# Kernel tuning notes

Measured on AMD Instinct MI355X. Metric: run time of the kernel, lower is better.

Reference implementation:

```python
import jax, jax.numpy as jnp
import numpy as np

T = 22        # TypeEncoder.tensor_size() (assumed)
H = 2         # attention heads
C = 64        # hc_graph (per-head out channels)
L = 3         # num_hops
LEAFCAT = 5   # len(LeafType.valid_categories()) (assumed)
NSIZES = 8    # len(LeafType.valid_sizes()) (assumed)
HL = 64       # hc_linear
HT = 64       # hc_task == hc_leafsize
SLOPE = 0.2   # PyG GATConv negative_slope


def _gat(x, src, dst, W, asrc, adst, b):
    # PyG GATConv (concat=True, dropout=0, self-loops already appended to src/dst)
    N = x.shape[0]
    h = (x @ W).reshape(N, H, C)                      # [N,H,C]
    a_s = jnp.einsum('nhc,hc->nh', h, asrc)            # per-node src score
    a_d = jnp.einsum('nhc,hc->nh', h, adst)            # per-node dst score
    e = jax.nn.leaky_relu(a_s[src] + a_d[dst], SLOPE)  # [E+N,H]
    m = jax.ops.segment_max(e, dst, num_segments=N)
    p = jnp.exp(e - m[dst])
    s = jax.ops.segment_sum(p, dst, num_segments=N)
    alpha = p / (s[dst] + 1e-16)                       # scatter-softmax over in-edges
    out = jax.ops.segment_sum(h[src] * alpha[:, :, None], dst, num_segments=N)
    return out.reshape(N, H * C) + b


def _mlp2(z, W1, b1, W2, b2):
    return jax.nn.relu(z @ W1 + b1) @ W2 + b2


def setup_inputs() -> dict:
    key = jax.random.key(0)
    ks = jax.random.split(key, 32)
    N, E, NG, NPG = 102400, 1228800, 256, 400
    D = H * C
    g = lambda k, shp, fan: (jax.random.normal(k, shp, jnp.float32) / np.sqrt(fan)).astype(jnp.float32)
    z = lambda *shp: jnp.zeros(shp, jnp.float32)
    return {
        'x': jax.random.normal(ks[0], (N, D), jnp.float32),
        'edge_index': jax.random.randint(ks[1], (2, E), 0, N),
        'batch': jnp.repeat(jnp.arange(NG, dtype=jnp.int32), NPG),
        'gat_W': g(ks[2], (L, D, D), D),
        'gat_asrc': g(ks[3], (L, H, C), C),
        'gat_adst': g(ks[4], (L, H, C), C),
        'gat_b': z(L, D),
        'shared_W': g(ks[5], (D + T, HL), D + T),
        'shared_b': z(HL),
        'ptr_W1': g(ks[6], (3, HL, HT), HL), 'ptr_b1': z(3, HT),
        'ptr_W2': g(ks[7], (3, HT, 3), HT), 'ptr_b2': z(3, 3),
        'cat_W1': g(ks[8], (HL, HT), HL), 'cat_b1': z(HT),
        'cat_W2': g(ks[9], (HT, LEAFCAT), HT), 'cat_b2': z(LEAFCAT),
        'sf_W1': g(ks[10], (2, HL, HT), HL), 'sf_b1': z(2, HT),
        'sf_W2': g(ks[11], (2, HT, 1), HT), 'sf_b2': z(2, 1),
        'bool_W1': g(ks[12], (HL + T + LEAFCAT + 2, HT), HL + T + LEAFCAT + 2), 'bool_b1': z(HT),
        'bool_W2': g(ks[13], (HT, 1), HT), 'bool_b2': z(1),
        'size_W1': g(ks[14], (HL + T + LEAFCAT + 3, HT), HL + T + LEAFCAT + 3), 'size_b1': z(HT),
        'size_W2': g(ks[15], (HT, NSIZES), HT), 'size_b2': z(NSIZES),
    }


def reference(x, edge_index, batch, gat_W, gat_asrc, gat_adst, gat_b,
              shared_W, shared_b, ptr_W1, ptr_b1, ptr_W2, ptr_b2,
              cat_W1, cat_b1, cat_W2, cat_b2, sf_W1, sf_b1, sf_W2, sf_b2,
              bool_W1, bool_b1, bool_W2, bool_b2, size_W1, size_b1, size_W2, size_b2):
    N = x.shape[0]
    num_graphs = int(batch[-1]) + 1                    # batch is sorted per-graph ids
    node0 = jnp.searchsorted(batch, jnp.arange(num_graphs))  # first node of each graph
    dtype_vec = x[node0, :T]                           # NodeEncoder.split_node_vec dtype slice
    loops = jnp.arange(N)
    src = jnp.concatenate([edge_index[0], loops])      # GATConv add_self_loops=True
    dst = jnp.concatenate([edge_index[1], loops])
    h = x
    for l in range(L):
        h = _gat(h, src, dst, gat_W[l], gat_asrc[l], gat_adst[l], gat_b[l])
        if l < L - 1:
            h = jax.nn.relu(h)
    zf = jax.nn.relu(jnp.concatenate([h[node0], dtype_vec], axis=1) @ shared_W + shared_b)
    # 3 pointer heads, batched
    p = jax.nn.relu(jnp.einsum('gh,khd->kgd', zf, ptr_W1) + ptr_b1[:, None, :])
    ptr = jnp.einsum('kgd,kdo->kgo', p, ptr_W2) + ptr_b2[:, None, :]
    cat_logits = _mlp2(zf, cat_W1, cat_b1, cat_W2, cat_b2)
    q = jax.nn.relu(jnp.einsum('gh,khd->kgd', zf, sf_W1) + sf_b1[:, None, :])
    sf = jnp.einsum('kgd,kdo->kgo', q, sf_W2) + sf_b2[:, None, :]
    signed, floating = sf[0], sf[1]
    bool_in = jnp.concatenate([zf, dtype_vec, cat_logits, signed, floating], axis=1)
    bool_logit = _mlp2(bool_in, bool_W1, bool_b1, bool_W2, bool_b2)
    size_in = jnp.concatenate([bool_in, bool_logit], axis=1)
    size_logits = _mlp2(size_in, size_W1, size_b1, size_W2, size_b2)
    return (ptr[0], ptr[1], ptr[2], cat_logits, signed, floating, bool_logit, size_logits)
```

## Files before the change

### kernel.cpp

```cpp
#include <hip/hip_runtime.h>
#include <hip/hip_bf16.h>

typedef __hip_bfloat16 bf16;
typedef __attribute__((ext_vector_type(8))) short short8;
typedef __attribute__((ext_vector_type(4))) float floatx4;

#define MF(a, b, c) __builtin_amdgcn_mfma_f32_16x16x32_bf16(a, b, c, 0, 0, 0)
#define ADJ_SLOTS 128

__device__ __forceinline__ float b2f(bf16 v) { return __bfloat162float(v); }
__device__ __forceinline__ unsigned short f2us(float f) {
    bf16 h = __float2bfloat16(f);
    return *(unsigned short*)&h;
}
__device__ __forceinline__ float lo2f(unsigned hv) { return __uint_as_float(hv << 16); }
__device__ __forceinline__ float hi2f(unsigned hv) { return __uint_as_float(hv & 0xffff0000u); }
__device__ __forceinline__ float leaky(float v) { return v > 0.f ? v : 0.2f * v; }

__device__ __forceinline__ float ldw(const void* p, size_t i, int f32) {
    return f32 ? ((const float*)p)[i] : b2f(((const bf16*)p)[i]);
}

template <int F32>
__device__ __forceinline__ float LDWt(const void* p, size_t i) {
    return F32 ? ((const float*)p)[i] : b2f(((const bf16*)p)[i]);
}

__device__ __forceinline__ void quadred(float part[4]) {
#pragma unroll
    for (int m = 1; m <= 8; m <<= 1)
#pragma unroll
        for (int r = 0; r < 4; r++) part[r] += __shfl_xor(part[r], m);
}

__global__ void k_detect_zero(const void* x, int* flagd, char* zbase, size_t zbytes,
                              const int* __restrict__ batch, int* __restrict__ node0,
                              unsigned char* __restrict__ rootb,
                              unsigned char* __restrict__ flag2, int N, int zBlocks) {
    int b = blockIdx.x;
    int t = threadIdx.x;
    if (b == 0) {
        __shared__ int sbad;
        if (t == 0) sbad = 0;
        __syncthreads();
        const bf16* xb = (const bf16*)x;
        int bad = 0;
#pragma unroll
        for (int j = 0; j < 16; j++) {
            float v = b2f(xb[t * 16 + j]);
            if (!(fabsf(v) < 1e10f)) bad = 1;
        }
        if (bad) sbad = 1;
        __syncthreads();
        if (t == 0) flagd[0] = sbad;
    } else if (b < 1 + zBlocks) {
        size_t off = (size_t)(b - 1) * 4096 + (size_t)t * 16;
        if (off < zbytes) *(uint4*)(zbase + off) = make_uint4(0u, 0u, 0u, 0u);
    } else {
        int i = (b - 1 - zBlocks) * 256 + t;
        if (i < N) {
            int bb = batch[i];
            int isroot = (i == 0) || (batch[i - 1] != bb);
            rootb[i] = (unsigned char)isroot;
            flag2[i] = (unsigned char)isroot;
            if (isroot) node0[bb] = i;
        }
    }
}

__global__ void k_prep(const void* __restrict__ x, unsigned short* __restrict__ Ab,
                       int nvec,
                       const void* __restrict__ gw, unsigned short* __restrict__ Wt,
                       const void* as_, const void* ad_, const void* b_,
                       float* asF, float* adF, float* bF,
                       const void* sW_, const void* pW1_, const void* cW1_,
                       const void* fW1_, const void* bW1_, const void* zW1_,
                       unsigned short* __restrict__ Whd,
                       const int* __restrict__ ei, const unsigned char* __restrict__ rootb,
                       unsigned char* __restrict__ flag2, int E,
                       const int* __restrict__ flagd, int nbE) {
    int b = blockIdx.x;
    int t = threadIdx.x;
    if (b < nbE) {
        int e = b * 256 + t;
        if (e < E && rootb[ei[E + e]]) flag2[ei[e]] = 1;
        return;
    }
    int f32 = *flagd;
    b -= nbE;
    if (b < 192) {
        int i = b * 256 + t;
        int l = i >> 14, rem = i & 16383, n = rem >> 7, k = rem & 127;
        Wt[i] = f2us(ldw(gw, (size_t)l * 16384 + (size_t)k * 128 + n, f32));
    } else if (b < 194) {
        int i = (b - 192) * 256 + t;
        if (i < 384) {
            asF[i] = ldw(as_, i, f32);
            adF[i] = ldw(ad_, i, f32);
            bF[i] = ldw(b_, i, f32);
        }
    } else if (b < 194 + 184) {
        int i = (b - 194) * 256 + t;
        float v;
        if (i < 10240) {
            int n = i / 160, k = i - n * 160;
            v = (k < 150) ? ldw(sW_, (size_t)k * 64 + n, f32) : 0.f;
        } else if (i < 22528) {
            int j = i - 10240;
            int kk = j >> 12, r = j & 4095, n = r >> 6, k = r & 63;
            v = ldw(pW1_, (size_t)kk * 4096 + (size_t)k * 64 + n, f32);
        } else if (i < 26624) {
            int j = i - 22528;
            int n = j >> 6, k = j & 63;
            v = ldw(cW1_, (size_t)k * 64 + n, f32);
        } else if (i < 34816) {
            int j = i - 26624;
            int kk = j >> 12, r = j & 4095, n = r >> 6, k = r & 63;
            v = ldw(fW1_, (size_t)kk * 4096 + (size_t)k * 64 + n, f32);
        } else if (i < 40960) {
            int j = i - 34816;
            int n = j / 96, k = j - n * 96;
            v = (k < 93) ? ldw(bW1_, (size_t)k * 64 + n, f32) : 0.f;
        } else {
            int j = i - 40960;
            int n = j / 96, k = j - n * 96;
            v = (k < 94) ? ldw(zW1_, (size_t)k * 64 + n, f32) : 0.f;
        }
        Whd[i] = f2us(v);
    } else {
        if (!f32) return;
        int i = (b - 194 - 184) * 256 + t;
        if (i < nvec) {
            float4 a = ((const float4*)x)[2 * i];
            float4 c = ((const float4*)x)[2 * i + 1];
            uint4 o;
            o.x = ((unsigned)f2us(a.y) << 16) | f2us(a.x);
            o.y = ((unsigned)f2us(a.w) << 16) | f2us(a.z);
            o.z = ((unsigned)f2us(c.y) << 16) | f2us(c.x);
            o.w = ((unsigned)f2us(c.w) << 16) | f2us(c.z);
            ((uint4*)Ab)[i] = o;
        }
    }
}

__global__ void k_scan2lane(const unsigned char* __restrict__ flag1,
                            const unsigned char* __restrict__ flag2,
                            int* __restrict__ wp1, int* __restrict__ wp2,
                            int* __restrict__ bsums, int* __restrict__ nact,
                            int* __restrict__ done, int n, int nb) {
    __shared__ int s[256];
    __shared__ int s2[512];
    __shared__ int lastFlag;
    int tid = threadIdx.x;
    int i = blockIdx.x * 256 + tid;
#pragma unroll
    for (int a = 0; a < 2; a++) {
        int v = 0;
        if (i < n) v = a == 0 ? (int)flag1[i] : (int)flag2[i];
        s[tid] = v;
        __syncthreads();
        for (int d = 1; d < 256; d <<= 1) {
            int t2 = (tid >= d) ? s[tid - d] : 0;
            __syncthreads();
            s[tid] += t2;
            __syncthreads();
        }
        int incl = s[tid];
        if (i < n) {
            if (a == 0) wp1[i] = incl - v;
            else wp2[i] = incl - v;
        }
        if (tid == 255) bsums[a * 512 + blockIdx.x] = incl;
        __syncthreads();
    }
    __threadfence();
    if (tid == 0) lastFlag = (atomicAdd(done, 1) == nb - 1);
    __syncthreads();
    if (!lastFlag) return;
    __threadfence();
#pragma unroll
    for (int a = 0; a < 2; a++) {
        int* arr = bsums + a * 512;
        int v0 = (tid < nb) ? arr[tid] : 0;
        int v1 = (tid + 256 < nb) ? arr[tid + 256] : 0;
        s2[tid] = v0;
        s2[tid + 256] = v1;
        __syncthreads();
        for (int d = 1; d < 512; d <<= 1) {
            int a0 = (tid >= d) ? s2[tid - d] : 0;
            int a1 = (tid + 256 >= d) ? s2[tid + 256 - d] : 0;
            __syncthreads();
            s2[tid] += a0;
            s2[tid + 256] += a1;
            __syncthreads();
        }
        arr[tid] = s2[tid] - v0;
        arr[tid + 256] = s2[tid + 256] - v1;
        if (tid == 255) nact[a] = s2[511];
        __syncthreads();
    }
}

__global__ void k_scatter_wl(const int* __restrict__ ei,
                             int* __restrict__ cur,
                             const unsigned char* __restrict__ flag1,
                             const unsigned char* __restrict__ flag2,
                             const int* __restrict__ wp1, const int* __restrict__ wp2,
                             const int* __restrict__ bsums,
                             int* __restrict__ adj,
                             int* __restrict__ ovfD, int* __restrict__ ovfS,
                             int* __restrict__ ovfCnt,
                             int* __restrict__ wl1, int* __restrict__ wl2,
                             int E, int N, int eBlocks) {
    int b = blockIdx.x;
    if (b < eBlocks) {
        int e = b * 256 + threadIdx.x;
        if (e >= E) return;
        int d = ei[E + e];
        if (!flag1[d]) return;
        int slot = atomicAdd(&cur[d], 1);
        if (slot < ADJ_SLOTS) {
            adj[(size_t)d * ADJ_SLOTS + slot] = ei[e];
        } else {
            int o = atomicAdd(ovfCnt, 1);
            if (o < E) { ovfD[o] = d; ovfS[o] = ei[e]; }
        }
    } else {
        int i = (b - eBlocks) * 256 + threadIdx.x;
        if (i < N) {
            if (flag1[i]) wl1[wp1[i] + bsums[i >> 8]] = i;
            if (flag2[i]) wl2[wp2[i] + bsums[512 + (i >> 8)]] = i;
        }
    }
}

__device__ __forceinline__ void gemm_body(
    const unsigned short* __restrict__ Asrc, const unsigned short* __restrict__ Wt,
    unsigned short* __restrict__ Bb, float4* __restrict__ asadv,
    const float* __restrict__ asF, const float* __restrict__ adF, int N,
    const int* __restrict__ wl, const int* __restrict__ nactp,
    int bb0, int bstride) {
    __shared__ __align__(16) unsigned short Ws[128 * 136];
    __shared__ __align__(16) unsigned short Cs[64 * 136];

    int t = threadIdx.x;
    int nact = wl ? *nactp : N;
    if (bb0 * 64 >= nact) return;

    {
        const uint4* src = (const uint4*)Wt;
#pragma unroll
        for (int k = 0; k < 8; k++) {
            int j = t + k * 256;
            int row = j >> 4, c16 = j & 15;
            *(uint4*)&Ws[row * 136 + c16 * 8] = src[j];
        }
    }
    __syncthreads();

    int lane = t & 63;
    int w = t >> 6;
    int ln = lane & 15;
    int quad = lane >> 4;

    for (int bb = bb0; bb * 64 < nact; bb += bstride) {
        int r0 = bb * 64;
        int idx = r0 + w * 16 + ln;
        bool valid = idx < nact;
        int arow = idx < N ? idx : N - 1;
        if (wl) arow = valid ? wl[idx] : 0;
        bool wave_active = __any((int)valid);

        if (wave_active) {
            const unsigned short* ap = Asrc + (size_t)arow * 128 + quad * 8;

            short8 afrag[4];
            if (valid) {
#pragma unroll
                for (int kt = 0; kt < 4; kt++)
                    afrag[kt] = *(const short8*)(ap + kt * 32);
            } else {
#pragma unroll
                for (int kt = 0; kt < 4; kt++)
                    afrag[kt] = (short8){0, 0, 0, 0, 0, 0, 0, 0};
            }

            floatx4 acc[8];
#pragma unroll
            for (int nt = 0; nt < 8; nt++) acc[nt] = (floatx4){0.f, 0.f, 0.f, 0.f};

#pragma unroll
            for (int nt = 0; nt < 8; nt++) {
                const unsigned short* wp = Ws + (nt * 16 + ln) * 136 + quad * 8;
#pragma unroll
                for (int kt = 0; kt < 4; kt++) {
                    short8 bfrag = *(const short8*)(wp + kt * 32);
                    acc[nt] = MF(afrag[kt], bfrag, acc[nt]);
                }
            }

            float as0[4] = {0, 0, 0, 0}, as1[4] = {0, 0, 0, 0};
            float ad0[4] = {0, 0, 0, 0}, ad1[4] = {0, 0, 0, 0};
#pragma unroll
            for (int nt = 0; nt < 8; nt++) {
                float asc = asF[nt * 16 + ln];
                float adc = adF[nt * 16 + ln];
#pragma unroll
                for (int r = 0; r < 4; r++) {
                    float v = acc[nt][r];
                    Cs[(w * 16 + quad * 4 + r) * 136 + nt * 16 + ln] = f2us(v);
                    if (nt < 4) { as0[r] += v * asc; ad0[r] += v * adc; }
                    else        { as1[r] += v * asc; ad1[r] += v * adc; }
                }
            }
#pragma unroll
            for (int mask = 1; mask <= 8; mask <<= 1) {
#pragma unroll
                for (int r = 0; r < 4; r++) {
                    as0[r] += __shfl_xor(as0[r], mask);
                    as1[r] += __shfl_xor(as1[r], mask);
                    ad0[r] += __shfl_xor(ad0[r], mask);
                    ad1[r] += __shfl_xor(ad1[r], mask);
                }
            }
            if (ln == 0) {
#pragma unroll
                for (int r = 0; r < 4; r++) {
                    int idx3 = r0 + w * 16 + quad * 4 + r;
                    if (idx3 < nact) {
                        int row = wl ? wl[idx3] : idx3;
                        asadv[row] = make_float4(as0[r], as1[r], ad0[r], ad1[r]);
                    }
                }
            }
        }
        __syncthreads();

        {
            int idx2 = r0 + (t >> 2);
            int cseg = (t & 3) * 32;
            if (idx2 < nact) {
                int grow = wl ? wl[idx2] : idx2;
                const short8* srcp = (const short8*)&Cs[(t >> 2) * 136 + cseg];
                short8* dstp = (short8*)&Bb[(size_t)grow * 128 + cseg];
#pragma unroll
                for (int u = 0; u < 4; u++) dstp[u] = srcp[u];
            }
        }
        __syncthreads();
    }
}

__global__ __launch_bounds__(256) void k_gemm_mfma(
    const unsigned short* __restrict__ Ab, const unsigned short* __restrict__ Wt,
    unsigned short* __restrict__ Bb, float4* __restrict__ asadv,
    const float* __restrict__ asF, const float* __restrict__ adF, int N,
    const int* __restrict__ wl, const int* __restrict__ nactp) {
    gemm_body(Ab, Wt, Bb, asadv, asF, adF, N, wl, nactp, blockIdx.x, gridDim.x);
}

__global__ __launch_bounds__(256) void k_gemm0_mark(
    const unsigned short* __restrict__ Ab, const void* __restrict__ xraw,
    const unsigned short* __restrict__ Wt,
    unsigned short* __restrict__ Bb, float4* __restrict__ asadv,
    const float* __restrict__ asF, const float* __restrict__ adF, int N,
    const int* __restrict__ ei, const unsigned char* __restrict__ flag2,
    unsigned char* __restrict__ flag1, int E, int markE, int markN,
    const int* __restrict__ flagd) {
    int b = blockIdx.x;
    if (b < markE) {
        int e = b * 256 + threadIdx.x;
        if (e < E && flag2[ei[E + e]]) flag1[ei[e]] = 1;
        return;
    }
    if (b < markE + markN) {
        int i = (b - markE) * 256 + threadIdx.x;
        if (i < N && flag2[i]) flag1[i] = 1;
        return;
    }
    const unsigned short* Asrc = *flagd ? Ab : (const unsigned short*)xraw;
    gemm_body(Asrc, Wt, Bb, asadv, asF, adF, N, nullptr, nullptr,
              b - markE - markN, gridDim.x - markE - markN);
}

__global__ void k_gat_agg(const uint2* __restrict__ Bu2, const float4* __restrict__ asadv,
                          const int* __restrict__ cur, const int* __restrict__ adj,
                          const int* __restrict__ ovfD, const int* __restrict__ ovfS,
                          const int* __restrict__ ovfCnt,
                          const float* __restrict__ biasF,
                          uint2* __restrict__ Au2,
                          const int* __restrict__ nactp, int nfix, int dorelu, int byidx,
                          const int* __restrict__ wl) {
    int totWaves = (gridDim.x * blockDim.x) >> 6;
    int wave0 = (blockIdx.x * blockDim.x + threadIdx.x) >> 6;
    int lane = threadIdx.x & 63;
    int hl = lane & 31;
    int hb = lane & 32;
    int half = lane >> 5;
    int head = hl >> 4;
    int n = nfix ? nfix : *nactp;

    for (int wv = wave0; wv * 2 < n; wv += totWaves) {
        int idx = wv * 2 + half;
        if (idx >= n) continue;
        int node = wl[idx];

        float4 self = asadv[node];
        float ad0 = self.z, ad1 = self.w;
        float es0 = __expf(leaky(self.x + ad0));
        float es1 = __expf(leaky(self.y + ad1));

        const int* ap = adj + (size_t)node * ADJ_SLOTS;
        int c = cur[node];
        uint2 hvs = Bu2[(size_t)node * 32 + hl];
        float acc0, acc1, acc2, acc3;

        if (c <= 32) {
            int src_r = 0;
            float p0 = 0.f, p1 = 0.f;
            if (hl < c) {
                src_r = ap[hl];
                float4 av = asadv[src_r];
                p0 = __expf(leaky(av.x + ad0));
                p1 = __expf(leaky(av.y + ad1));
            }
            float t0 = p0, t1 = p1;
#pragma unroll
            for (int mask = 1; mask <= 16; mask <<= 1) {
                t0 += __shfl_xor(t0, mask);
                t1 += __shfl_xor(t1, mask);
            }
            float inv0 = 1.f / (es0 + t0 + 1e-16f);
            float inv1 = 1.f / (es1 + t1 + 1e-16f);
            p0 *= inv0;
            p1 *= inv1;
            float aself = head ? es1 * inv1 : es0 * inv0;
            acc0 = aself * lo2f(hvs.x);
            acc1 = aself * hi2f(hvs.x);
            acc2 = aself * lo2f(hvs.y);
            acc3 = aself * hi2f(hvs.y);

            uint2 hq[4];
#pragma unroll
            for (int j = 0; j < 4; j++) {
                int s2 = __shfl(src_r, hb + j);
                hq[j] = make_uint2(0u, 0u);
                if (j < c) hq[j] = Bu2[(size_t)s2 * 32 + hl];
            }

            for (int base = 0; base < c; base += 4) {
                uint2 cu[4];
                float av4[4];
#pragma unroll
                for (int j = 0; j < 4; j++) {
                    cu[j] = hq[j];
                    int idx2 = (base + j) & 31;
                    float a0 = __shfl(p0, hb + idx2);
                    float a1 = __shfl(p1, hb + idx2);
                    float a = head ? a1 : a0;
                    av4[j] = (base + j < c) ? a : 0.f;
                }
#pragma unroll
                for (int j = 0; j < 4; j++) {
                    int nx = base + 4 + j;
                    int s2 = __shfl(src_r, hb + (nx & 31));
                    if (nx < c) hq[j] = Bu2[(size_t)s2 * 32 + hl];
                }
#pragma unroll
                for (int j = 0; j < 4; j++) {
                    acc0 += av4[j] * lo2f(cu[j].x);
                    acc1 += av4[j] * hi2f(cu[j].x);
                    acc2 += av4[j] * lo2f(cu[j].y);
                    acc3 += av4[j] * hi2f(cu[j].y);
                }
            }
        } else {
            float sum0 = es0, sum1 = es1;
            int cc = min(c, ADJ_SLOTS);
            for (int base = 0; base < cc; base += 32) {
                int i = base + hl;
                float p0 = 0.f, p1 = 0.f;
                if (i < cc) {
                    int s = ap[i];
                    float4 av = asadv[s];
                    p0 = __expf(leaky(av.x + ad0));
                    p1 = __expf(leaky(av.y + ad1));
                }
                float t0 = p0, t1 = p1;
#pragma unroll
                for (int mask = 1; mask <= 16; mask <<= 1) {
                    t0 += __shfl_xor(t0, mask);
                    t1 += __shfl_xor(t1, mask);
                }
                sum0 += t0; sum1 += t1;
            }
            int no = (c > ADJ_SLOTS) ? *ovfCnt : 0;
            for (int oe = 0; oe < no; oe++) {
                if (ovfD[oe] == node) {
                    float4 av = asadv[ovfS[oe]];
                    sum0 += __expf(leaky(av.x + ad0));
                    sum1 += __expf(leaky(av.y + ad1));
                }
            }
            float inv0 = 1.f / (sum0 + 1e-16f);
            float inv1 = 1.f / (sum1 + 1e-16f);
            float aself = head ? es1 * inv1 : es0 * inv0;
            float invh = head ? inv1 : inv0;
            acc0 = aself * lo2f(hvs.x);
            acc1 = aself * hi2f(hvs.x);
            acc2 = aself * lo2f(hvs.y);
            acc3 = aself * hi2f(hvs.y);
            for (int i = 0; i < cc; i++) {
                int s = ap[i];
                float4 av = asadv[s];
                float a = (head ? __expf(leaky(av.y + ad1)) : __expf(leaky(av.x + ad0))) * invh;
                uint2 hv = Bu2[(size_t)s * 32 + hl];
                acc0 += a * lo2f(hv.x);
                acc1 += a * hi2f(hv.x);
                acc2 += a * lo2f(hv.y);
                acc3 += a * hi2f(hv.y);
            }
            for (int oe = 0; oe < no; oe++) {
                if (ovfD[oe] == node) {
                    int s = ovfS[oe];
                    float4 av = asadv[s];
                    float a = (head ? __expf(leaky(av.y + ad1)) : __expf(leaky(av.x + ad0))) * invh;
                    uint2 hv = Bu2[(size_t)s * 32 + hl];
                    acc0 += a * lo2f(hv.x);
                    acc1 += a * hi2f(hv.x);
                    acc2 += a * lo2f(hv.y);
                    acc3 += a * hi2f(hv.y);
                }
            }
        }

        float4 bb4 = ((const float4*)biasF)[hl];
        float q0 = acc0 + bb4.x;
        float q1 = acc1 + bb4.y;
        float q2 = acc2 + bb4.z;
        float q3 = acc3 + bb4.w;
        if (dorelu) {
            q0 = fmaxf(q0, 0.f); q1 = fmaxf(q1, 0.f);
            q2 = fmaxf(q2, 0.f); q3 = fmaxf(q3, 0.f);
        }
        Au2[(size_t)(byidx ? idx : node) * 32 + hl] =
            make_uint2(((unsigned)f2us(q1) << 16) | f2us(q0),
                       ((unsigned)f2us(q3) << 16) | f2us(q2));
    }
}

template <int F32>
__device__ void heads_mfma_body(
    const unsigned* __restrict__ hroot32, const void* __restrict__ x,
    const int* __restrict__ node0, const unsigned short* __restrict__ Whd,
    const void* sb, const void* pb1, const void* pW2, const void* pb2,
    const void* cb1, const void* cW2, const void* cb2,
    const void* fb1, const void* fW2, const void* fb2,
    const void* bb1, const void* bW2, const void* bb2,
    const void* zb1, const void* zW2, const void* zb2,
    void* __restrict__ outv) {
    __shared__ __align__(16) unsigned short hinS[64 * 168];
    __shared__ __align__(16) unsigned short TwS[4][16 * 168];

    int t = threadIdx.x;
    int g0b = blockIdx.x * 64;
    bf16* outb = (bf16*)outv;
    float* outf = (float*)outv;
#define STORE(idx, val) do { if (F32) outf[idx] = (val); else outb[idx] = __float2bfloat16(val); } while (0)

    {
        unsigned* h32 = (unsigned*)hinS;
        for (int j = t; j < 64 * 64; j += 256) {
            int gl = j >> 6, c = j & 63;
            h32[gl * 84 + c] = hroot32[(size_t)(g0b + gl) * 64 + c];
        }
        for (int j = t; j < 64 * 20; j += 256) {
            int gl = j / 20, c = j - gl * 20;
            int n0 = node0[g0b + gl];
            int k0 = 2 * c;
            float d0 = (k0 < 22) ? LDWt<F32>(x, (size_t)n0 * 128 + k0) : 0.f;
            float d1 = (k0 + 1 < 22) ? LDWt<F32>(x, (size_t)n0 * 128 + k0 + 1) : 0.f;
            h32[gl * 84 + 64 + c] = ((unsigned)f2us(d1) << 16) | f2us(d0);
        }
    }
    __syncthreads();

    int w = t >> 6;
    int lane = t & 63;
    int ln = lane & 15, quad = lane >> 4;
    unsigned short* T = TwS[w];
    int gq = quad * 4;
    int gw0 = g0b + w * 16;

    for (int j = lane; j < 16 * 32; j += 64) {
        int gl = j >> 5, c = j & 31;
        T[gl * 168 + 64 + c] =
            (c < 22) ? hinS[(w * 16 + gl) * 168 + 128 + c] : (unsigned short)0;
    }

    short8 afA[5];
#pragma unroll
    for (int kt = 0; kt < 5; kt++)
        afA[kt] = *(const short8*)&hinS[(w * 16 + ln) * 168 + quad * 8 + kt * 32];
#pragma unroll
    for (int nt = 0; nt < 4; nt++) {
        floatx4 acc = (floatx4){0.f, 0.f, 0.f, 0.f};
        const unsigned short* bp = Whd + (nt * 16 + ln) * 160 + quad * 8;
#pragma unroll
        for (int kt = 0; kt < 5; kt++)
            acc = MF(afA[kt], *(const short8*)(bp + kt * 32), acc);
        float bias = LDWt<F32>(sb, nt * 16 + ln);
#pragma unroll
        for (int r = 0; r < 4; r++)
            T[(gq + r) * 168 + nt * 16 + ln] = f2us(fmaxf(acc[r] + bias, 0.f));
    }
    __syncthreads();

    short8 af20 = *(const short8*)&T[ln * 168 + quad * 8];
    short8 af21 = *(const short8*)&T[ln * 168 + quad * 8 + 32];

#pragma unroll
    for (int k = 0; k < 3; k++) {
        const unsigned short* Bw = Whd + 10240 + k * 4096;
        floatx4 acc[4];
#pragma unroll
        for (int nt = 0; nt < 4; nt++) {
            floatx4 a = (floatx4){0.f, 0.f, 0.f, 0.f};
            const unsigned short* bp = Bw + (nt * 16 + ln) * 64 + quad * 8;
            a = MF(af20, *(const short8*)bp, a);
            a = MF(af21, *(const short8*)(bp + 32), a);
            float b1 = LDWt<F32>(pb1, k * 64 + nt * 16 + ln);
#pragma unroll
            for (int r = 0; r < 4; r++) a[r] = fmaxf(a[r] + b1, 0.f);
            acc[nt] = a;
        }
#pragma unroll
        for (int o = 0; o < 3; o++) {
            float w2[4], part[4];
#pragma unroll
            for (int nt = 0; nt < 4; nt++)
                w2[nt] = LDWt<F32>(pW2, (size_t)k * 192 + (size_t)(nt * 16 + ln) * 3 + o);
#pragma unroll
            for (int r = 0; r < 4; r++)
                part[r] = acc[0][r] * w2[0] + acc[1][r] * w2[1] +
                          acc[2][r] * w2[2] + acc[3][r] * w2[3];
            quadred(part);
            if (ln == 0) {
                float b2 = LDWt<F32>(pb2, k * 3 + o);
#pragma unroll
                for (int r = 0; r < 4; r++)
                    STORE(k * 768 + (gw0 + gq + r) * 3 + o, part[r] + b2);
            }
        }
    }

    {
        const unsigned short* Bw = Whd + 22528;
        floatx4 acc[4];
#pragma unroll
        for (int nt = 0; nt < 4; nt++) {
            floatx4 a = (floatx4){0.f, 0.f, 0.f, 0.f};
            const unsigned short* bp = Bw + (nt * 16 + ln) * 64 + quad * 8;
            a = MF(af20, *(const short8*)bp, a);
            a = MF(af21, *(const short8*)(bp + 32), a);
            float b1 = LDWt<F32>(cb1, nt * 16 + ln);
#pragma unroll
            for (int r = 0; r < 4; r++) a[r] = fmaxf(a[r] + b1, 0.f);
            acc[nt] = a;
        }
#pragma unroll
        for (int o = 0; o < 5; o++) {
            float w2[4], part[4];
#pragma unroll
            for (int nt = 0; nt < 4; nt++)
                w2[nt] = LDWt<F32>(cW2, (size_t)(nt * 16 + ln) * 5 + o);
#pragma unroll
            for (int r = 0; r < 4; r++)
                part[r] = acc[0][r] * w2[0] + acc[1][r] * w2[1] +
                          acc[2][r] * w2[2] + acc[3][r] * w2[3];
            quadred(part);
            if (ln == 0) {
                float b2 = LDWt<F32>(cb2, o);
#pragma unroll
                for (int r = 0; r < 4; r++) {
                    float v = part[r] + b2;
                    T[(gq + r) * 168 + 86 + o] = f2us(v);
                    STORE(2304 + (gw0 + gq + r) * 5 + o, v);
                }
            }
        }
    }

#pragma unroll
    for (int k = 0; k < 2; k++) {
        const unsigned short* Bw = Whd + 26624 + k * 4096;
        floatx4 acc[4];
#pragma unroll
        for (int nt = 0; nt < 4; nt++) {
            floatx4 a = (floatx4){0.f, 0.f, 0.f, 0.f};
            const unsigned short* bp = Bw + (nt * 16 + ln) * 64 + quad * 8;
            a = MF(af20, *(const short8*)bp, a);
            a = MF(af21, *(const short8*)(bp + 32), a);
            float b1 = LDWt<F32>(fb1, k * 64 + nt * 16 + ln);
#pragma unroll
            for (int r = 0; r < 4; r++) a[r] = fmaxf(a[r] + b1, 0.f);
            acc[nt] = a;
        }
        float w2[4], part[4];
#pragma unroll
        for (int nt = 0; nt < 4; nt++)
            w2[nt] = LDWt<F32>(fW2, (size_t)k * 64 + nt * 16 + ln);
#pragma unroll
        for (int r = 0; r < 4; r++)
            part[r] = acc[0][r] * w2[0] + acc[1][r] * w2[1] +
                      acc[2][r] * w2[2] + acc[3][r] * w2[3];
        quadred(part);
        if (ln == 0) {
            float b2 = LDWt<F32>(fb2, k);
#pragma unroll
            for (int r = 0; r < 4; r++) {
                float v = part[r] + b2;
                T[(gq + r) * 168 + 91 + k] = f2us(v);
                STORE(3584 + k * 256 + (gw0 + gq + r), v);
            }
        }
    }
    __syncthreads();

    short8 af3 = *(const short8*)&T[ln * 168 + 64 + quad * 8];

    {
        const unsigned short* Bw = Whd + 34816;
        floatx4 acc[4];
#pragma unroll
        for (int nt = 0; nt < 4; nt++) {
            floatx4 a = (floatx4){0.f, 0.f, 0.f, 0.f};
            const unsigned short* bp = Bw + (nt * 16 + ln) * 96 + quad * 8;
            a = MF(af20, *(const short8*)bp, a);
            a = MF(af21, *(const short8*)(bp + 32), a);
            a = MF(af3, *(const short8*)(bp + 64), a);
            float b1 = LDWt<F32>(bb1, nt * 16 + ln);
#pragma unroll
            for (int r = 0; r < 4; r++) a[r] = fmaxf(a[r] + b1, 0.f);
            acc[nt] = a;
        }
        float w2[4], part[4];
#pragma unroll
        for (int nt = 0; nt < 4; nt++)
            w2[nt] = LDWt<F32>(bW2, nt * 16 + ln);
#pragma unroll
        for (int r = 0; r < 4; r++)
            part[r] = acc[0][r] * w2[0] + acc[1][r] * w2[1] +
                      acc[2][r] * w2[2] + acc[3][r] * w2[3];
        quadred(part);
        if (ln == 0) {
            float b2 = LDWt<F32>(bb2, 0);
#pragma unroll
            for (int r = 0; r < 4; r++) {
                float v = part[r] + b2;
                T[(gq + r) * 168 + 93] = f2us(v);
                STORE(4096 + (gw0 + gq + r), v);
            }
        }
    }
    __syncthreads();

    af3 = *(const short8*)&T[ln * 168 + 64 + quad * 8];

    {
        const unsigned short* Bw = Whd + 40960;
        floatx4 acc[4];
#pragma unroll
        for (int nt = 0; nt < 4; nt++) {
            floatx4 a = (floatx4){0.f, 0.f, 0.f, 0.f};
            const unsigned short* bp = Bw + (nt * 16 + ln) * 96 + quad * 8;
            a = MF(af20, *(const short8*)bp, a);
            a = MF(af21, *(const short8*)(bp + 32), a);
            a = MF(af3, *(const short8*)(bp + 64), a);
            float b1 = LDWt<F32>(zb1, nt * 16 + ln);
#pragma unroll
            for (int r = 0; r < 4; r++) a[r] = fmaxf(a[r] + b1, 0.f);
            acc[nt] = a;
        }
#pragma unroll
        for (int o = 0; o < 8; o++) {
            float w2[4], part[4];
#pragma unroll
            for (int nt = 0; nt < 4; nt++)
                w2[nt] = LDWt<F32>(zW2, (size_t)(nt * 16 + ln) * 8 + o);
#pragma unroll
            for (int r = 0; r < 4; r++)
                part[r] = acc[0][r] * w2[0] + acc[1][r] * w2[1] +
                          acc[2][r] * w2[2] + acc[3][r] * w2[3];
            quadred(part);
            if (ln == 0) {
                float b2 = LDWt<F32>(zb2, o);
#pragma unroll
                for (int r = 0; r < 4; r++)
                    STORE(4352 + (gw0 + gq + r) * 8 + o, part[r] + b2);
            }
        }
    }
#undef STORE
}

__global__ __launch_bounds__(256) void k_heads_mfma(
    const unsigned* __restrict__ hroot32, const void* __restrict__ x,
    const int* __restrict__ node0, const unsigned short* __restrict__ Whd,
    const void* sb, const void* pb1, const void* pW2, const void* pb2,
    const void* cb1, const void* cW2, const void* cb2,
    const void* fb1, const void* fW2, const void* fb2,
    const void* bb1, const void* bW2, const void* bb2,
    const void* zb1, const void* zW2, const void* zb2,
    void* __restrict__ outv, const int* __restrict__ flagd) {
    if (*flagd)
        heads_mfma_body<1>(hroot32, x, node0, Whd, sb, pb1, pW2, pb2, cb1, cW2, cb2,
                           fb1, fW2, fb2, bb1, bW2, bb2, zb1, zW2, zb2, outv);
    else
        heads_mfma_body<0>(hroot32, x, node0, Whd, sb, pb1, pW2, pb2, cb1, cW2, cb2,
                           fb1, fW2, fb2, bb1, bW2, bb2, zb1, zW2, zb2, outv);
}


extern "C" void kernel_launch(void* const* d_in, const int* in_sizes, int n_in,
                              void* d_out, int out_size, void* d_ws, size_t ws_size,
                              hipStream_t stream) {
    const void* x     = d_in[0];
    const int*  ei    = (const int*)d_in[1];
    const int*  batch = (const int*)d_in[2];

    int N = in_sizes[0] / 128;
    int E = in_sizes[1] / 2;

    char* w = (char*)d_ws;
    float4* asad = (float4*)w;              w += (size_t)N * 16;
    unsigned short* A = (unsigned short*)w; w += (size_t)N * 128 * 2;
    unsigned short* B = (unsigned short*)w; w += (size_t)N * 128 * 2;
    unsigned short* Wt = (unsigned short*)w; w += 3 * 16384 * 2;
    unsigned short* Whd = (unsigned short*)w; w += 47104 * 2;
    float* asF = (float*)w;                 w += 384 * 4;
    float* adF = (float*)w;                 w += 384 * 4;
    float* bF = (float*)w;                  w += 384 * 4;
    int* wp1 = (int*)w;                     w += (size_t)N * 4;
    int* wp2 = (int*)w;                     w += (size_t)N * 4;
    int* wl1 = (int*)w;                     w += (size_t)N * 4;
    int* wl2 = (int*)w;                     w += (size_t)N * 4;
    int* adj = (int*)w;                     w += (size_t)N * ADJ_SLOTS * 4;
    int* ovfD = (int*)w;                    w += (size_t)E * 4;
    int* ovfS = (int*)w;                    w += (size_t)E * 4;
    int* bsums = (int*)w;                   w += 3 * 512 * 4;
    int* node0 = (int*)w;                   w += 256 * 4;
    int* nact = (int*)w;                    w += 64;
    unsigned* hroot = (unsigned*)w;         w += 256 * 128 * 2;
    char* zbase = w;
    int* cur = (int*)w;                     w += (size_t)N * 4;
    unsigned char* flag1 = (unsigned char*)w; w += (size_t)N;
    int* done = (int*)w;                    w += 64;
    int* ovfCnt = (int*)w;                  w += 64;
    size_t zbytes = (size_t)N * 5 + 128;
    int* flagd = (int*)w;                   w += 64;
    unsigned char* rootb = (unsigned char*)w; w += (size_t)N;
    unsigned char* flag2 = (unsigned char*)w; w += (size_t)N;

    int nb = (N + 255) / 256;
    int nvec = N * 16;
    int nbx8 = (nvec + 255) / 256;
    int nbE = (E + 255) / 256;
    int zBlocks = (int)((zbytes + 4095) / 4096);

    k_detect_zero<<<1 + zBlocks + nb, 256, 0, stream>>>(
        x, flagd, zbase, zbytes, batch, node0, rootb, flag2, N, zBlocks);

    k_prep<<<nbE + 194 + 184 + nbx8, 256, 0, stream>>>(
        x, A, nvec, d_in[3], Wt, d_in[4], d_in[5], d_in[6],
        asF, adF, bF,
        d_in[7], d_in[9], d_in[13], d_in[17], d_in[21], d_in[25], Whd,
        ei, rootb, flag2, E, flagd, nbE);

    k_gemm0_mark<<<nbE + nb + 800, 256, 0, stream>>>(
        A, x, Wt, B, asad, asF, adF, N, ei, flag2, flag1, E, nbE, nb, flagd);

    k_scan2lane<<<nb, 256, 0, stream>>>(flag1, flag2, wp1, wp2, bsums, nact, done, N, nb);

    k_scatter_wl<<<nbE + nb, 256, 0, stream>>>(
        ei, cur, flag1, flag2, wp1, wp2, bsums, adj, ovfD, ovfS, ovfCnt,
        wl1, wl2, E, N, nbE);

    k_gat_agg<<<2048, 256, 0, stream>>>(
        (const uint2*)B, asad, cur, adj, ovfD, ovfS, ovfCnt, bF, (uint2*)A,
        nact, 0, 1, 0, wl1);

    k_gemm_mfma<<<512, 256, 0, stream>>>(
        A, Wt + 16384, B, asad, asF + 128, adF + 128, N, wl1, nact);

    k_gat_agg<<<512, 256, 0, stream>>>(
        (const uint2*)B, asad, cur, adj, ovfD, ovfS, ovfCnt, bF + 128, (uint2*)A,
        nact + 1, 0, 1, 0, wl2);

    k_gemm_mfma<<<128, 256, 0, stream>>>(
        A, Wt + 2 * 16384, B, asad, asF + 256, adF + 256, N, wl2, nact + 1);

    k_gat_agg<<<32, 256, 0, stream>>>(
        (const uint2*)B, asad, cur, adj, ovfD, ovfS, ovfCnt, bF + 256, (uint2*)hroot,
        nact, 256, 0, 1, node0);

    k_heads_mfma<<<4, 256, 0, stream>>>(
        hroot, x, node0, Whd,
        d_in[8], d_in[10], d_in[11], d_in[12],
        d_in[14], d_in[15], d_in[16],
        d_in[18], d_in[19], d_in[20],
        d_in[22], d_in[23], d_in[24],
        d_in[26], d_in[27], d_in[28],
        d_out, flagd);
}
```

Baseline: 320.7 us.

## Replace prefix-scan worklist with atomic append and fuse root aggregation into heads

Removes the two-lane prefix scan kernel and builds the active-node worklists with atomic counters in the scatter kernel, so worklist order becomes nondeterministic. Also drops the final root-node GAT aggregation launch by computing that aggregation inside the heads kernel, writing results straight to shared memory instead of a global hroot buffer. This cuts two kernel launches and a scan pass, at the cost of atomic contention on two counters and serial aggregation inside the 4-block heads kernel.

```diff
diff --git a/kernel.cpp b/kernel.cpp
--- a/kernel.cpp
+++ b/kernel.cpp
@@ -143,74 +143,15 @@
     }
 }
 
-__global__ void k_scan2lane(const unsigned char* __restrict__ flag1,
-                            const unsigned char* __restrict__ flag2,
-                            int* __restrict__ wp1, int* __restrict__ wp2,
-                            int* __restrict__ bsums, int* __restrict__ nact,
-                            int* __restrict__ done, int n, int nb) {
-    __shared__ int s[256];
-    __shared__ int s2[512];
-    __shared__ int lastFlag;
-    int tid = threadIdx.x;
-    int i = blockIdx.x * 256 + tid;
-#pragma unroll
-    for (int a = 0; a < 2; a++) {
-        int v = 0;
-        if (i < n) v = a == 0 ? (int)flag1[i] : (int)flag2[i];
-        s[tid] = v;
-        __syncthreads();
-        for (int d = 1; d < 256; d <<= 1) {
-            int t2 = (tid >= d) ? s[tid - d] : 0;
-            __syncthreads();
-            s[tid] += t2;
-            __syncthreads();
-        }
-        int incl = s[tid];
-        if (i < n) {
-            if (a == 0) wp1[i] = incl - v;
-            else wp2[i] = incl - v;
-        }
-        if (tid == 255) bsums[a * 512 + blockIdx.x] = incl;
-        __syncthreads();
-    }
-    __threadfence();
-    if (tid == 0) lastFlag = (atomicAdd(done, 1) == nb - 1);
-    __syncthreads();
-    if (!lastFlag) return;
-    __threadfence();
-#pragma unroll
-    for (int a = 0; a < 2; a++) {
-        int* arr = bsums + a * 512;
-        int v0 = (tid < nb) ? arr[tid] : 0;
-        int v1 = (tid + 256 < nb) ? arr[tid + 256] : 0;
-        s2[tid] = v0;
-        s2[tid + 256] = v1;
-        __syncthreads();
-        for (int d = 1; d < 512; d <<= 1) {
-            int a0 = (tid >= d) ? s2[tid - d] : 0;
-            int a1 = (tid + 256 >= d) ? s2[tid + 256 - d] : 0;
-            __syncthreads();
-            s2[tid] += a0;
-            s2[tid + 256] += a1;
-            __syncthreads();
-        }
-        arr[tid] = s2[tid] - v0;
-        arr[tid + 256] = s2[tid + 256] - v1;
-        if (tid == 255) nact[a] = s2[511];
-        __syncthreads();
-    }
-}
-
 __global__ void k_scatter_wl(const int* __restrict__ ei,
                              int* __restrict__ cur,
                              const unsigned char* __restrict__ flag1,
                              const unsigned char* __restrict__ flag2,
-                             const int* __restrict__ wp1, const int* __restrict__ wp2,
-                             const int* __restrict__ bsums,
                              int* __restrict__ adj,
                              int* __restrict__ ovfD, int* __restrict__ ovfS,
                              int* __restrict__ ovfCnt,
                              int* __restrict__ wl1, int* __restrict__ wl2,
+                             int* __restrict__ nactp,
                              int E, int N, int eBlocks) {
     int b = blockIdx.x;
     if (b < eBlocks) {
@@ -228,8 +169,8 @@
     } else {
         int i = (b - eBlocks) * 256 + threadIdx.x;
         if (i < N) {
-            if (flag1[i]) wl1[wp1[i] + bsums[i >> 8]] = i;
-            if (flag2[i]) wl2[wp2[i] + bsums[512 + (i >> 8)]] = i;
+            if (flag1[i]) wl1[atomicAdd(&nactp[0], 1)] = i;
+            if (flag2[i]) wl2[atomicAdd(&nactp[32], 1)] = i;
         }
     }
 }
@@ -389,7 +330,7 @@
                           const int* __restrict__ ovfCnt,
                           const float* __restrict__ biasF,
                           uint2* __restrict__ Au2,
-                          const int* __restrict__ nactp, int nfix, int dorelu, int byidx,
+                          const int* __restrict__ nactp, int dorelu,
                           const int* __restrict__ wl) {
     int totWaves = (gridDim.x * blockDim.x) >> 6;
     int wave0 = (blockIdx.x * blockDim.x + threadIdx.x) >> 6;
@@ -398,7 +339,7 @@
     int hb = lane & 32;
     int half = lane >> 5;
     int head = hl >> 4;
-    int n = nfix ? nfix : *nactp;
+    int n = *nactp;
 
     for (int wv = wave0; wv * 2 < n; wv += totWaves) {
         int idx = wv * 2 + half;
@@ -543,7 +484,7 @@
             q0 = fmaxf(q0, 0.f); q1 = fmaxf(q1, 0.f);
             q2 = fmaxf(q2, 0.f); q3 = fmaxf(q3, 0.f);
         }
-        Au2[(size_t)(byidx ? idx : node) * 32 + hl] =
+        Au2[(size_t)node * 32 + hl] =
             make_uint2(((unsigned)f2us(q1) << 16) | f2us(q0),
                        ((unsigned)f2us(q3) << 16) | f2us(q2));
     }
@@ -551,7 +492,11 @@
 
 template <int F32>
 __device__ void heads_mfma_body(
-    const unsigned* __restrict__ hroot32, const void* __restrict__ x,
+    const uint2* __restrict__ Bu2, const float4* __restrict__ asadv,
+    const int* __restrict__ cur, const int* __restrict__ adj,
+    const int* __restrict__ ovfD, const int* __restrict__ ovfS,
+    const int* __restrict__ ovfCnt, const float* __restrict__ biasF,
+    const void* __restrict__ x,
     const int* __restrict__ node0, const unsigned short* __restrict__ Whd,
     const void* sb, const void* pb1, const void* pW2, const void* pb2,
     const void* cb1, const void* cW2, const void* cb2,
@@ -568,26 +513,140 @@
     float* outf = (float*)outv;
 #define STORE(idx, val) do { if (F32) outf[idx] = (val); else outb[idx] = __float2bfloat16(val); } while (0)
 
-    {
-        unsigned* h32 = (unsigned*)hinS;
-        for (int j = t; j < 64 * 64; j += 256) {
-            int gl = j >> 6, c = j & 63;
-            h32[gl * 84 + c] = hroot32[(size_t)(g0b + gl) * 64 + c];
-        }
-        for (int j = t; j < 64 * 20; j += 256) {
-            int gl = j / 20, c = j - gl * 20;
-            int n0 = node0[g0b + gl];
-            int k0 = 2 * c;
-            float d0 = (k0 < 22) ? LDWt<F32>(x, (size_t)n0 * 128 + k0) : 0.f;
-            float d1 = (k0 + 1 < 22) ? LDWt<F32>(x, (size_t)n0 * 128 + k0 + 1) : 0.f;
-            h32[gl * 84 + 64 + c] = ((unsigned)f2us(d1) << 16) | f2us(d0);
-        }
-    }
-    __syncthreads();
-
     int w = t >> 6;
     int lane = t & 63;
+    int hl = lane & 31;
+    int hb = lane & 32;
+    int half = lane >> 5;
+    int head = hl >> 4;
     int ln = lane & 15, quad = lane >> 4;
+    unsigned* h32 = (unsigned*)hinS;
+
+    for (int j = t; j < 64 * 20; j += 256) {
+        int gl = j / 20, c = j - gl * 20;
+        int n0 = node0[g0b + gl];
+        int k0 = 2 * c;
+        float d0 = (k0 < 22) ? LDWt<F32>(x, (size_t)n0 * 128 + k0) : 0.f;
+        float d1 = (k0 + 1 < 22) ? LDWt<F32>(x, (size_t)n0 * 128 + k0 + 1) : 0.f;
+        h32[gl * 84 + 64 + c] = ((unsigned)f2us(d1) << 16) | f2us(d0);
+    }
+
+    for (int pr = 0; pr < 8; ++pr) {
+        int gl = w * 16 + pr * 2 + half;
+        int node = node0[g0b + gl];
+
+        float4 self = asadv[node];
+        float ad0 = self.z, ad1 = self.w;
+        float es0 = __expf(leaky(self.x + ad0));
+        float es1 = __expf(leaky(self.y + ad1));
+        const int* ap = adj + (size_t)node * ADJ_SLOTS;
+        int c = cur[node];
+        uint2 hvs = Bu2[(size_t)node * 32 + hl];
+        float acc0, acc1, acc2, acc3;
+
+        if (c <= 32) {
+            int src_r = 0;
+            float p0 = 0.f, p1 = 0.f;
+            if (hl < c) {
+                src_r = ap[hl];
+                float4 av = asadv[src_r];
+                p0 = __expf(leaky(av.x + ad0));
+                p1 = __expf(leaky(av.y + ad1));
+            }
+            float t0 = p0, t1 = p1;
+#pragma unroll
+            for (int mask = 1; mask <= 16; mask <<= 1) {
+                t0 += __shfl_xor(t0, mask);
+                t1 += __shfl_xor(t1, mask);
+            }
+            float inv0 = 1.f / (es0 + t0 + 1e-16f);
+            float inv1 = 1.f / (es1 + t1 + 1e-16f);
+            p0 *= inv0;
+            p1 *= inv1;
+            float aself = head ? es1 * inv1 : es0 * inv0;
+            acc0 = aself * lo2f(hvs.x);
+            acc1 = aself * hi2f(hvs.x);
+            acc2 = aself * lo2f(hvs.y);
+            acc3 = aself * hi2f(hvs.y);
+            for (int j = 0; j < c; j++) {
+                int s2 = __shfl(src_r, hb + j);
+                float a0 = __shfl(p0, hb + j);
+                float a1 = __shfl(p1, hb + j);
+                float a = head ? a1 : a0;
+                uint2 hv = Bu2[(size_t)s2 * 32 + hl];
+                acc0 += a * lo2f(hv.x);
+                acc1 += a * hi2f(hv.x);
+                acc2 += a * lo2f(hv.y);
+                acc3 += a * hi2f(hv.y);
+            }
+        } else {
+            float sum0 = es0, sum1 = es1;
+            int cc = min(c, ADJ_SLOTS);
+            for (int base = 0; base < cc; base += 32) {
+                int i = base + hl;
+                float p0 = 0.f, p1 = 0.f;
+                if (i < cc) {
+                    int s = ap[i];
+                    float4 av = asadv[s];
+                    p0 = __expf(leaky(av.x + ad0));
+                    p1 = __expf(leaky(av.y + ad1));
+                }
+                float t0 = p0, t1 = p1;
+#pragma unroll
+                for (int mask = 1; mask <= 16; mask <<= 1) {
+                    t0 += __shfl_xor(t0, mask);
+                    t1 += __shfl_xor(t1, mask);
+                }
+                sum0 += t0; sum1 += t1;
+            }
+            int no = (c > ADJ_SLOTS) ? *ovfCnt : 0;
+            for (int oe = 0; oe < no; oe++) {
+                if (ovfD[oe] == node) {
+                    float4 av = asadv[ovfS[oe]];
+                    sum0 += __expf(leaky(av.x + ad0));
+                    sum1 += __expf(leaky(av.y + ad1));
+                }
+            }
+            float inv0 = 1.f / (sum0 + 1e-16f);
+            float inv1 = 1.f / (sum1 + 1e-16f);
+            float aself = head ? es1 * inv1 : es0 * inv0;
+            float invh = head ? inv1 : inv0;
+            acc0 = aself * lo2f(hvs.x);
+            acc1 = aself * hi2f(hvs.x);
+            acc2 = aself * lo2f(hvs.y);
+            acc3 = aself * hi2f(hvs.y);
+            for (int i = 0; i < cc; i++) {
+                int s = ap[i];
+                float4 av = asadv[s];
+                float a = (head ? __expf(leaky(av.y + ad1)) : __expf(leaky(av.x + ad0))) * invh;
+                uint2 hv = Bu2[(size_t)s * 32 + hl];
+                acc0 += a * lo2f(hv.x);
+                acc1 += a * hi2f(hv.x);
+                acc2 += a * lo2f(hv.y);
+                acc3 += a * hi2f(hv.y);
+            }
+            for (int oe = 0; oe < no; oe++) {
+                if (ovfD[oe] == node) {
+                    int s = ovfS[oe];
+                    float4 av = asadv[s];
+                    float a = (head ? __expf(leaky(av.y + ad1)) : __expf(leaky(av.x + ad0))) * invh;
+                    uint2 hv = Bu2[(size_t)s * 32 + hl];
+                    acc0 += a * lo2f(hv.x);
+                    acc1 += a * hi2f(hv.x);
+                    acc2 += a * lo2f(hv.y);
+                    acc3 += a * hi2f(hv.y);
+                }
+            }
+        }
+
+        float4 bb4 = ((const float4*)biasF)[hl];
+        h32[gl * 84 + 2 * hl] =
+            ((unsigned)f2us(acc1 + bb4.y) << 16) | f2us(acc0 + bb4.x);
+        h32[gl * 84 + 2 * hl + 1] =
+            ((unsigned)f2us(acc3 + bb4.w) << 16) | f2us(acc2 + bb4.z);
+    }
+    __syncthreads();
+
     unsigned short* T = TwS[w];
     int gq = quad * 4;
     int gw0 = g0b + w * 16;
@@ -805,7 +864,11 @@
 }
 
 __global__ __launch_bounds__(256) void k_heads_mfma(
-    const unsigned* __restrict__ hroot32, const void* __restrict__ x,
+    const uint2* __restrict__ Bu2, const float4* __restrict__ asadv,
+    const int* __restrict__ cur, const int* __restrict__ adj,
+    const int* __restrict__ ovfD, const int* __restrict__ ovfS,
+    const int* __restrict__ ovfCnt, const float* __restrict__ biasF,
+    const void* __restrict__ x,
     const int* __restrict__ node0, const unsigned short* __restrict__ Whd,
     const void* sb, const void* pb1, const void* pW2, const void* pb2,
     const void* cb1, const void* cW2, const void* cb2,
@@ -814,10 +877,12 @@
     const void* zb1, const void* zW2, const void* zb2,
     void* __restrict__ outv, const int* __restrict__ flagd) {
     if (*flagd)
-        heads_mfma_body<1>(hroot32, x, node0, Whd, sb, pb1, pW2, pb2, cb1, cW2, cb2,
+        heads_mfma_body<1>(Bu2, asadv, cur, adj, ovfD, ovfS, ovfCnt, biasF, x,
+                           node0, Whd, sb, pb1, pW2, pb2, cb1, cW2, cb2,
                            fb1, fW2, fb2, bb1, bW2, bb2, zb1, zW2, zb2, outv);
     else
-        heads_mfma_body<0>(hroot32, x, node0, Whd, sb, pb1, pW2, pb2, cb1, cW2, cb2,
+        heads_mfma_body<0>(Bu2, asadv, cur, adj, ovfD, ovfS, ovfCnt, biasF, x,
+                           node0, Whd, sb, pb1, pW2, pb2, cb1, cW2, cb2,
                            fb1, fW2, fb2, bb1, bW2, bb2, zb1, zW2, zb2, outv);
 }
 
@@ -841,23 +906,18 @@
     float* asF = (float*)w;                 w += 384 * 4;
     float* adF = (float*)w;                 w += 384 * 4;
     float* bF = (float*)w;                  w += 384 * 4;
-    int* wp1 = (int*)w;                     w += (size_t)N * 4;
-    int* wp2 = (int*)w;                     w += (size_t)N * 4;
     int* wl1 = (int*)w;                     w += (size_t)N * 4;
     int* wl2 = (int*)w;                     w += (size_t)N * 4;
     int* adj = (int*)w;                     w += (size_t)N * ADJ_SLOTS * 4;
     int* ovfD = (int*)w;                    w += (size_t)E * 4;
     int* ovfS = (int*)w;                    w += (size_t)E * 4;
-    int* bsums = (int*)w;                   w += 3 * 512 * 4;
     int* node0 = (int*)w;                   w += 256 * 4;
-    int* nact = (int*)w;                    w += 64;
-    unsigned* hroot = (unsigned*)w;         w += 256 * 128 * 2;
     char* zbase = w;
     int* cur = (int*)w;                     w += (size_t)N * 4;
     unsigned char* flag1 = (unsigned char*)w; w += (size_t)N;
-    int* done = (int*)w;                    w += 64;
+    int* nact = (int*)w;                    w += 64 * 4;
     int* ovfCnt = (int*)w;                  w += 64;
-    size_t zbytes = (size_t)N * 5 + 128;
+    size_t zbytes = (size_t)N * 5 + 64 * 4 + 64;
     int* flagd = (int*)w;                   w += 64;
     unsigned char* rootb = (unsigned char*)w; w += (size_t)N;
     unsigned char* flag2 = (unsigned char*)w; w += (size_t)N;
@@ -880,32 +940,25 @@
     k_gemm0_mark<<<nbE + nb + 800, 256, 0, stream>>>(
         A, x, Wt, B, asad, asF, adF, N, ei, flag2, flag1, E, nbE, nb, flagd);
 
-    k_scan2lane<<<nb, 256, 0, stream>>>(flag1, flag2, wp1, wp2, bsums, nact, done, N, nb);
-
     k_scatter_wl<<<nbE + nb, 256, 0, stream>>>(
-        ei, cur, flag1, flag2, wp1, wp2, bsums, adj, ovfD, ovfS, ovfCnt,
-        wl1, wl2, E, N, nbE);
+        ei, cur, flag1, flag2, adj, ovfD, ovfS, ovfCnt, wl1, wl2, nact, E, N, nbE);
 
     k_gat_agg<<<2048, 256, 0, stream>>>(
         (const uint2*)B, asad, cur, adj, ovfD, ovfS, ovfCnt, bF, (uint2*)A,
-        nact, 0, 1, 0, wl1);
+        nact, 1, wl1);
 
     k_gemm_mfma<<<512, 256, 0, stream>>>(
         A, Wt + 16384, B, asad, asF + 128, adF + 128, N, wl1, nact);
 
     k_gat_agg<<<512, 256, 0, stream>>>(
         (const uint2*)B, asad, cur, adj, ovfD, ovfS, ovfCnt, bF + 128, (uint2*)A,
-        nact + 1, 0, 1, 0, wl2);
+        nact + 32, 1, wl2);
 
     k_gemm_mfma<<<128, 256, 0, stream>>>(
-        A, Wt + 2 * 16384, B, asad, asF + 256, adF + 256, N, wl2, nact + 1);
-
-    k_gat_agg<<<32, 256, 0, stream>>>(
-        (const uint2*)B, asad, cur, adj, ovfD, ovfS, ovfCnt, bF + 256, (uint2*)hroot,
-        nact, 256, 0, 1, node0);
+        A, Wt + 2 * 16384, B, asad, asF + 256, adF + 256, N, wl2, nact + 32);
 
     k_heads_mfma<<<4, 256, 0, stream>>>(
-        hroot, x, node0, Whd,
+        (const uint2*)B, asad, cur, adj, ovfD, ovfS, ovfCnt, bF + 256, x, node0, Whd,
         d_in[8], d_in[10], d_in[11], d_in[12],
         d_in[14], d_in[15], d_in[16],
         d_in[18], d_in[19], d_in[20],
```

New measurement: 352.6 us. 1.1x slower.
